# Optimization experiments

Measured on AMD Instinct MI355X. Metric: run time of the kernel, lower is better.

## Reference

```python
import jax, jax.numpy as jnp
import numpy as np

B, S, D = 16, 4096, 64
DROPOUT_KEY = jax.random.key(1)


def setup_inputs() -> dict:
    key = jax.random.key(0)
    kq, kk, kv = jax.random.split(key, 3)
    return {
        "query": jax.random.normal(kq, (B, S, D), dtype=jnp.float32),
        "key": jax.random.normal(kk, (B, S, D), dtype=jnp.float32),
        "value": jax.random.normal(kv, (B, S, D), dtype=jnp.float32),
        "dropout_p": jnp.float32(0.01),
        "inv_scale_factor": jnp.float32(8.0),  # sqrt(head_dim)
    }


def reference(query, key, value, dropout_p, inv_scale_factor):
    # scores: [B, Sq, Skv]
    scores = jnp.einsum("bqd,bkd->bqk", query, key) / inv_scale_factor
    attn = jax.nn.softmax(scores, axis=-1)
    # deterministic dropout with a fixed key (faithful train-mode dropout)
    keep = jax.random.bernoulli(DROPOUT_KEY, 1.0 - dropout_p, attn.shape)
    attn = jnp.where(keep, attn / (1.0 - dropout_p), 0.0)
    return jnp.einsum("bqk,bkd->bqd", attn, value)
```

## Files before the change

### kernel.cpp

```cpp
#include <hip/hip_runtime.h>
#include <stdint.h>


typedef _Float16 half4 __attribute__((ext_vector_type(4)));
typedef _Float16 half8 __attribute__((ext_vector_type(8)));
typedef float    f32x4 __attribute__((ext_vector_type(4)));

#if defined(__has_builtin)
#if __has_builtin(__builtin_amdgcn_exp2f)
#define EXP2(x) __builtin_amdgcn_exp2f(x)
#else
#define EXP2(x) exp2f(x)
#endif
#else
#define EXP2(x) exp2f(x)
#endif

#define ROTL(x, r) (((x) << (r)) | ((x) >> (32 - (r))))

__device__ __forceinline__ uint32_t tf2x32_xor(uint32_t n) {
  const uint32_t ks2 = 0x1BD11BDBu;
  uint32_t x0 = 0u, x1 = n;
#define TFR(r) { x0 += x1; x1 = ROTL(x1, r); x1 ^= x0; }
  x1 += 1u;
  TFR(13) TFR(15) TFR(26) TFR(6)
  x0 += 1u;  x1 += ks2 + 1u;
  TFR(17) TFR(29) TFR(16) TFR(24)
  x0 += ks2; x1 += 2u;
  TFR(13) TFR(15) TFR(26) TFR(6)
  x1 += 4u;
  TFR(17) TFR(29) TFR(16) TFR(24)
  x0 += 1u;  x1 += ks2 + 4u;
  TFR(13) TFR(15) TFR(26) TFR(6)
  x0 += ks2; x1 += 5u;
#undef TFR
  return x0 ^ x1;
}

__device__ __forceinline__ float jax_uniform(uint32_t w) {
  return __uint_as_float((w >> 9) | 0x3f800000u) - 1.0f;
}


__global__ void cvt_qk_kernel(const float* __restrict__ q,
                              const float* __restrict__ k,
                              const float* __restrict__ inv_scale,
                              _Float16* __restrict__ qh,
                              _Float16* __restrict__ kh) {
  const int tid = blockIdx.x * 256 + threadIdx.x;
  const int half_t = 1048576;
  const float qs = 1.4426950408889634f / inv_scale[0];
  if (tid < half_t) {
    float4 d = *(const float4*)(q + (size_t)tid * 4);
    half4 h = { (_Float16)(d.x * qs), (_Float16)(d.y * qs),
                (_Float16)(d.z * qs), (_Float16)(d.w * qs) };
    *(half4*)(qh + (size_t)tid * 4) = h;
  } else {
    const int t2 = tid - half_t;
    float4 d = *(const float4*)(k + (size_t)t2 * 4);
    half4 h = { (_Float16)d.x, (_Float16)d.y, (_Float16)d.z, (_Float16)d.w };
    *(half4*)(kh + (size_t)t2 * 4) = h;
  }
}

__global__ void cvt_v_kernel(const float* __restrict__ v,
                             _Float16* __restrict__ vt) {
  __shared__ float tile[64][65];
  const int b  = blockIdx.x >> 6;
  const int st = blockIdx.x & 63;
  const int t  = threadIdx.x;
  const float* src = v + ((size_t)b * 4096 + (size_t)st * 64) * 64;
#pragma unroll
  for (int i = 0; i < 4; ++i) {
    const int r = i * 16 + (t >> 4);
    const int c = (t & 15) * 4;
    float4 d = *(const float4*)(src + r * 64 + c);
    tile[r][c] = d.x; tile[r][c + 1] = d.y; tile[r][c + 2] = d.z; tile[r][c + 3] = d.w;
  }
  __syncthreads();
  _Float16* dst = vt + (size_t)b * 64 * 4096 + (size_t)st * 64;
#pragma unroll
  for (int i = 0; i < 4; ++i) {
    const int d0 = i * 16 + (t >> 4);
    const int s0 = (t & 15) * 4;
    half4 h = { (_Float16)tile[s0][d0],     (_Float16)tile[s0 + 1][d0],
                (_Float16)tile[s0 + 2][d0], (_Float16)tile[s0 + 3][d0] };
    *(half4*)(dst + (size_t)d0 * 4096 + s0) = h;
  }
}

__global__ __launch_bounds__(256, 2) void flash_attn(
    const _Float16* __restrict__ qh,
    const _Float16* __restrict__ kh,
    const _Float16* __restrict__ vth,
    const float* __restrict__ dropout_p,
    float* __restrict__ out) {
  __shared__ alignas(16) _Float16 Kt[2][64 * 72];
  __shared__ alignas(16) _Float16 Vt[2][64 * 72];
  __shared__ float Lrow[2][64];

  const int pair = blockIdx.x & 7;
  const int q0   = (blockIdx.x >> 3) * 64;
  const int wave = threadIdx.x >> 6;
  const int lane = threadIdx.x & 63;
  const int l15  = lane & 15;
  const int l4   = lane >> 4;

  const float keep_p = 1.0f - dropout_p[0];

  half8 qfrag[2][2];
#pragma unroll
  for (int b2 = 0; b2 < 2; ++b2) {
    const _Float16* qp = qh +
        (((size_t)(pair + 8 * b2) * 4096 + q0 + 16 * wave + l15) * 64 + l4 * 8);
    qfrag[b2][0] = *(const half8*)qp;
    qfrag[b2][1] = *(const half8*)(qp + 32);
  }

  const f32x4 Zv = {0.f, 0.f, 0.f, 0.f};
  f32x4 oacc[2][4];
#pragma unroll
  for (int b2 = 0; b2 < 2; ++b2)
#pragma unroll
    for (int t = 0; t < 4; ++t) oacc[b2][t] = Zv;
  float lpart[2] = {0.f, 0.f};

  const uint32_t nlo = ((uint32_t)pair << 24) +
                       ((uint32_t)(q0 + 16 * wave + l15) << 12) +
                       (uint32_t)(4 * l4);

  for (int step = 0; step < 64; ++step) {
    const int key0 = step * 64;
    __syncthreads();
#pragma unroll
    for (int b2 = 0; b2 < 2; ++b2) {
      const _Float16* kb = kh + ((size_t)(pair + 8 * b2) * 4096 + key0) * 64;
      const _Float16* vb = vth + (size_t)(pair + 8 * b2) * 64 * 4096 + key0;
#pragma unroll
      for (int i = 0; i < 2; ++i) {
        const int chunk = threadIdx.x + i * 256;
        const int row = chunk >> 3;
        const int c   = (chunk & 7) * 8;
        *(half8*)&Kt[b2][row * 72 + c] = *(const half8*)(kb + row * 64 + c);
        *(half8*)&Vt[b2][row * 72 + c] = *(const half8*)(vb + (size_t)row * 4096 + c);
      }
    }
    __syncthreads();

    f32x4 sacc[2][4];
#pragma unroll
    for (int b2 = 0; b2 < 2; ++b2)
#pragma unroll
      for (int t = 0; t < 4; ++t) {
        sacc[b2][t] = Zv;
#pragma unroll
        for (int s = 0; s < 2; ++s) {
          half8 kf = *(const half8*)&Kt[b2][(16 * t + l15) * 72 + l4 * 8 + s * 32];
          sacc[b2][t] = __builtin_amdgcn_mfma_f32_16x16x32_f16(
              kf, qfrag[b2][s], sacc[b2][t], 0, 0, 0);
        }
      }

#pragma unroll
    for (int t = 0; t < 4; ++t) {
      const uint32_t cb = nlo + (uint32_t)(key0 + 16 * t);
      half4 pf[2];
#pragma unroll
      for (int r = 0; r < 4; ++r) {
        const uint32_t n = cb + (uint32_t)r;
        const uint32_t w0 = tf2x32_xor(n);
        const uint32_t w1 = tf2x32_xor(n + 0x08000000u);
        const float p0 = EXP2(sacc[0][t][r]);
        const float p1 = EXP2(sacc[1][t][r]);
        lpart[0] += p0;
        lpart[1] += p1;
        pf[0][r] = (_Float16)((jax_uniform(w0) < keep_p) ? p0 : 0.0f);
        pf[1][r] = (_Float16)((jax_uniform(w1) < keep_p) ? p1 : 0.0f);
      }
#pragma unroll
      for (int b2 = 0; b2 < 2; ++b2)
#pragma unroll
        for (int t2 = 0; t2 < 4; ++t2) {
          half4 vf = *(const half4*)&Vt[b2][(16 * t2 + l15) * 72 + 16 * t + 4 * l4];
          oacc[b2][t2] = __builtin_amdgcn_mfma_f32_16x16x16f16(
              pf[b2], vf, oacc[b2][t2], 0, 0, 0);
        }
    }
  }

#pragma unroll
  for (int b2 = 0; b2 < 2; ++b2) {
    float l = lpart[b2];
    l += __shfl_xor(l, 16, 64);
    l += __shfl_xor(l, 32, 64);
    if (lane < 16) Lrow[b2][16 * wave + lane] = l;
  }
  __syncthreads();
  float inv[2][4];
#pragma unroll
  for (int b2 = 0; b2 < 2; ++b2)
#pragma unroll
    for (int r = 0; r < 4; ++r)
      inv[b2][r] = 1.0f / (keep_p * Lrow[b2][16 * wave + 4 * l4 + r]);
#pragma unroll
  for (int b2 = 0; b2 < 2; ++b2)
#pragma unroll
    for (int t2 = 0; t2 < 4; ++t2)
#pragma unroll
      for (int r = 0; r < 4; ++r)
        out[((size_t)(pair + 8 * b2) * 4096 + q0 + 16 * wave + 4 * l4 + r) * 64 +
            16 * t2 + l15] = oacc[b2][t2][r] * inv[b2][r];
}


extern "C" void kernel_launch(void* const* d_in, const int* in_sizes, int n_in,
                              void* d_out, int out_size, void* d_ws, size_t ws_size,
                              hipStream_t stream) {
  const float* q   = (const float*)d_in[0];
  const float* k   = (const float*)d_in[1];
  const float* v   = (const float*)d_in[2];
  const float* dp  = (const float*)d_in[3];
  const float* isf = (const float*)d_in[4];
  float* out = (float*)d_out;

  const size_t N = (size_t)16 * 4096 * 64;
  _Float16* qh  = (_Float16*)d_ws;
  _Float16* kh  = qh + N;
  _Float16* vth = kh + N;

  cvt_qk_kernel<<<8192, 256, 0, stream>>>(q, k, isf, qh, kh);
  cvt_v_kernel<<<1024, 256, 0, stream>>>(v, vth);
  flash_attn<<<512, 256, 0, stream>>>(qh, kh, vth, dp, out);
}
```

Before: 674.5 us.

## Split batch pair across waves, halve query tile, and use integer dropout compare

Each wave now handles one batch of the pair (wave&1) for 16 query rows, with 32 queries per block, so the grid doubles to 1024 blocks and each thread's register state drops by half. Launch bounds are raised to 4 blocks per CU to allow more occupancy. The dropout test becomes a direct integer comparison against a precomputed threshold, and the rotate uses alignbit. The cost is that K/V tiles are now loaded into shared memory twice as often per query row, so global and LDS traffic per unit of output rises.

```diff
diff --git a/kernel.cpp b/kernel.cpp
--- a/kernel.cpp
+++ b/kernel.cpp
@@ -16,7 +16,7 @@
 #define EXP2(x) exp2f(x)
 #endif
 
-#define ROTL(x, r) (((x) << (r)) | ((x) >> (32 - (r))))
+#define ROTL(x, r) __builtin_amdgcn_alignbit((x), (x), 32 - (r))
 
 __device__ __forceinline__ uint32_t tf2x32_xor(uint32_t n) {
   const uint32_t ks2 = 0x1BD11BDBu;
@@ -35,10 +35,6 @@
   x0 += ks2; x1 += 5u;
 #undef TFR
   return x0 ^ x1;
-}
-
-__device__ __forceinline__ float jax_uniform(uint32_t w) {
-  return __uint_as_float((w >> 9) | 0x3f800000u) - 1.0f;
 }
 
 
@@ -89,7 +85,7 @@
   }
 }
 
-__global__ __launch_bounds__(256, 2) void flash_attn(
+__global__ __launch_bounds__(256, 4) void flash_attn(
     const _Float16* __restrict__ qh,
     const _Float16* __restrict__ kh,
     const _Float16* __restrict__ vth,
@@ -97,119 +93,93 @@
     float* __restrict__ out) {
   __shared__ alignas(16) _Float16 Kt[2][64 * 72];
   __shared__ alignas(16) _Float16 Vt[2][64 * 72];
-  __shared__ float Lrow[2][64];
 
   const int pair = blockIdx.x & 7;
-  const int q0   = (blockIdx.x >> 3) * 64;
+  const int q0   = (blockIdx.x >> 3) * 32;
   const int wave = threadIdx.x >> 6;
   const int lane = threadIdx.x & 63;
   const int l15  = lane & 15;
   const int l4   = lane >> 4;
+  const int b2   = wave & 1;
+  const int qw   = (wave >> 1) * 16;
+  const int batch = pair + 8 * b2;
 
   const float keep_p = 1.0f - dropout_p[0];
-
-  half8 qfrag[2][2];
-#pragma unroll
-  for (int b2 = 0; b2 < 2; ++b2) {
-    const _Float16* qp = qh +
-        (((size_t)(pair + 8 * b2) * 4096 + q0 + 16 * wave + l15) * 64 + l4 * 8);
-    qfrag[b2][0] = *(const half8*)qp;
-    qfrag[b2][1] = *(const half8*)(qp + 32);
-  }
+  const uint32_t thr = (uint32_t)ceilf(keep_p * 8388608.0f);
+  const uint32_t thr9 = (thr >= 8388608u) ? 0xFFFFFFFFu : (thr << 9);
+
+  const _Float16* qp = qh +
+      (((size_t)batch * 4096 + q0 + qw + l15) * 64 + l4 * 8);
+  const half8 qfrag0 = *(const half8*)qp;
+  const half8 qfrag1 = *(const half8*)(qp + 32);
 
   const f32x4 Zv = {0.f, 0.f, 0.f, 0.f};
-  f32x4 oacc[2][4];
-#pragma unroll
-  for (int b2 = 0; b2 < 2; ++b2)
-#pragma unroll
-    for (int t = 0; t < 4; ++t) oacc[b2][t] = Zv;
-  float lpart[2] = {0.f, 0.f};
-
-  const uint32_t nlo = ((uint32_t)pair << 24) +
-                       ((uint32_t)(q0 + 16 * wave + l15) << 12) +
+  f32x4 oacc[4] = {Zv, Zv, Zv, Zv};
+  float lpart = 0.f;
+
+  const uint32_t nlo = ((uint32_t)batch << 24) +
+                       ((uint32_t)(q0 + qw + l15) << 12) +
                        (uint32_t)(4 * l4);
 
   for (int step = 0; step < 64; ++step) {
     const int key0 = step * 64;
     __syncthreads();
 #pragma unroll
-    for (int b2 = 0; b2 < 2; ++b2) {
-      const _Float16* kb = kh + ((size_t)(pair + 8 * b2) * 4096 + key0) * 64;
-      const _Float16* vb = vth + (size_t)(pair + 8 * b2) * 64 * 4096 + key0;
+    for (int bb = 0; bb < 2; ++bb) {
+      const _Float16* kb = kh + ((size_t)(pair + 8 * bb) * 4096 + key0) * 64;
+      const _Float16* vb = vth + (size_t)(pair + 8 * bb) * 64 * 4096 + key0;
 #pragma unroll
       for (int i = 0; i < 2; ++i) {
         const int chunk = threadIdx.x + i * 256;
         const int row = chunk >> 3;
         const int c   = (chunk & 7) * 8;
-        *(half8*)&Kt[b2][row * 72 + c] = *(const half8*)(kb + row * 64 + c);
-        *(half8*)&Vt[b2][row * 72 + c] = *(const half8*)(vb + (size_t)row * 4096 + c);
+        *(half8*)&Kt[bb][row * 72 + c] = *(const half8*)(kb + row * 64 + c);
+        *(half8*)&Vt[bb][row * 72 + c] = *(const half8*)(vb + (size_t)row * 4096 + c);
       }
     }
     __syncthreads();
 
-    f32x4 sacc[2][4];
-#pragma unroll
-    for (int b2 = 0; b2 < 2; ++b2)
-#pragma unroll
-      for (int t = 0; t < 4; ++t) {
-        sacc[b2][t] = Zv;
-#pragma unroll
-        for (int s = 0; s < 2; ++s) {
-          half8 kf = *(const half8*)&Kt[b2][(16 * t + l15) * 72 + l4 * 8 + s * 32];
-          sacc[b2][t] = __builtin_amdgcn_mfma_f32_16x16x32_f16(
-              kf, qfrag[b2][s], sacc[b2][t], 0, 0, 0);
-        }
-      }
+    f32x4 sacc[4];
+#pragma unroll
+    for (int t = 0; t < 4; ++t) {
+      const half8 kf0 = *(const half8*)&Kt[b2][(16 * t + l15) * 72 + l4 * 8];
+      const half8 kf1 = *(const half8*)&Kt[b2][(16 * t + l15) * 72 + l4 * 8 + 32];
+      sacc[t] = __builtin_amdgcn_mfma_f32_16x16x32_f16(kf0, qfrag0, Zv, 0, 0, 0);
+      sacc[t] = __builtin_amdgcn_mfma_f32_16x16x32_f16(kf1, qfrag1, sacc[t], 0, 0, 0);
+    }
 
 #pragma unroll
     for (int t = 0; t < 4; ++t) {
       const uint32_t cb = nlo + (uint32_t)(key0 + 16 * t);
-      half4 pf[2];
+      half4 pf;
 #pragma unroll
       for (int r = 0; r < 4; ++r) {
-        const uint32_t n = cb + (uint32_t)r;
-        const uint32_t w0 = tf2x32_xor(n);
-        const uint32_t w1 = tf2x32_xor(n + 0x08000000u);
-        const float p0 = EXP2(sacc[0][t][r]);
-        const float p1 = EXP2(sacc[1][t][r]);
-        lpart[0] += p0;
-        lpart[1] += p1;
-        pf[0][r] = (_Float16)((jax_uniform(w0) < keep_p) ? p0 : 0.0f);
-        pf[1][r] = (_Float16)((jax_uniform(w1) < keep_p) ? p1 : 0.0f);
+        const uint32_t w = tf2x32_xor(cb + (uint32_t)r);
+        const float p = EXP2(sacc[t][r]);
+        lpart += p;
+        pf[r] = (_Float16)((w < thr9) ? p : 0.0f);
       }
 #pragma unroll
-      for (int b2 = 0; b2 < 2; ++b2)
-#pragma unroll
-        for (int t2 = 0; t2 < 4; ++t2) {
-          half4 vf = *(const half4*)&Vt[b2][(16 * t2 + l15) * 72 + 16 * t + 4 * l4];
-          oacc[b2][t2] = __builtin_amdgcn_mfma_f32_16x16x16f16(
-              pf[b2], vf, oacc[b2][t2], 0, 0, 0);
-        }
+      for (int t2 = 0; t2 < 4; ++t2) {
+        const half4 vf = *(const half4*)&Vt[b2][(16 * t2 + l15) * 72 + 16 * t + 4 * l4];
+        oacc[t2] = __builtin_amdgcn_mfma_f32_16x16x16f16(pf, vf, oacc[t2], 0, 0, 0);
+      }
     }
   }
 
-#pragma unroll
-  for (int b2 = 0; b2 < 2; ++b2) {
-    float l = lpart[b2];
-    l += __shfl_xor(l, 16, 64);
-    l += __shfl_xor(l, 32, 64);
-    if (lane < 16) Lrow[b2][16 * wave + lane] = l;
-  }
-  __syncthreads();
-  float inv[2][4];
-#pragma unroll
-  for (int b2 = 0; b2 < 2; ++b2)
+  float l = lpart;
+  l += __shfl_xor(l, 16, 64);
+  l += __shfl_xor(l, 32, 64);
+  float inv[4];
+#pragma unroll
+  for (int r = 0; r < 4; ++r)
+    inv[r] = 1.0f / (keep_p * __shfl(l, 4 * l4 + r, 64));
+#pragma unroll
+  for (int t2 = 0; t2 < 4; ++t2)
 #pragma unroll
     for (int r = 0; r < 4; ++r)
-      inv[b2][r] = 1.0f / (keep_p * Lrow[b2][16 * wave + 4 * l4 + r]);
-#pragma unroll
-  for (int b2 = 0; b2 < 2; ++b2)
-#pragma unroll
-    for (int t2 = 0; t2 < 4; ++t2)
-#pragma unroll
-      for (int r = 0; r < 4; ++r)
-        out[((size_t)(pair + 8 * b2) * 4096 + q0 + 16 * wave + 4 * l4 + r) * 64 +
-            16 * t2 + l15] = oacc[b2][t2][r] * inv[b2][r];
+      out[((size_t)batch * 4096 + q0 + qw + 4 * l4 + r) * 64 + 16 * t2 + l15] =
+          oacc[t2][r] * inv[r];
 }
 
 
@@ -230,5 +200,5 @@
 
   cvt_qk_kernel<<<8192, 256, 0, stream>>>(q, k, isf, qh, kh);
   cvt_v_kernel<<<1024, 256, 0, stream>>>(v, vth);
-  flash_attn<<<512, 256, 0, stream>>>(qh, kh, vth, dp, out);
-}
+  flash_attn<<<1024, 256, 0, stream>>>(qh, kh, vth, dp, out);
+}
```

Measured after the change: 625.6 us. 7.2% less time.
